# Performance work log

Hardware: AMD Instinct MI355X
Metric: run time of the kernel (lower is better)

Reference implementation:

```python
import jax, jax.numpy as jnp
import numpy as np

V = 25000
E = 100000
NODE_IN = 74
EDGE_IN = 12
OUT = 64
EHID = 128
NUM_STEPS = 6


def setup_inputs() -> dict:
    key = jax.random.key(0)
    ks = jax.random.split(key, 12)
    s = 0.05
    node_feats = jax.random.normal(ks[0], (V, NODE_IN), dtype=jnp.float32)
    edge_feats = jax.random.normal(ks[1], (E, EDGE_IN), dtype=jnp.float32)
    src = jax.random.randint(ks[2], (E,), 0, V)
    dst = jax.random.randint(ks[3], (E,), 0, V)
    # project_node_feats: Linear(node_in, out)
    Wp = jax.random.normal(ks[4], (NODE_IN, OUT), dtype=jnp.float32) * s
    bp = jnp.zeros((OUT,), dtype=jnp.float32)
    # edge network: Linear(edge_in, ehid) -> ReLU -> Linear(ehid, out*out)
    We1 = jax.random.normal(ks[5], (EDGE_IN, EHID), dtype=jnp.float32) * s
    be1 = jnp.zeros((EHID,), dtype=jnp.float32)
    We2 = jax.random.normal(ks[6], (EHID, OUT * OUT), dtype=jnp.float32) * s
    be2 = jnp.zeros((OUT * OUT,), dtype=jnp.float32)
    # NNConv output bias
    bias = jnp.zeros((OUT,), dtype=jnp.float32)
    return {
        "node_feats": node_feats, "edge_feats": edge_feats,
        "src": src, "dst": dst,
        "Wp": Wp, "bp": bp,
        "We1": We1, "be1": be1, "We2": We2, "be2": be2,
        "bias": bias,
    }


def reference(node_feats, edge_feats, src, dst, Wp, bp, We1, be1, We2, be2, bias):
    # project node features
    h = jax.nn.relu(node_feats @ Wp + bp)  # [V, OUT]
    # per-edge weight matrices (same every step -> hoist out of loop)
    ew = jax.nn.relu(edge_feats @ We1 + be1) @ We2 + be2  # [E, OUT*OUT]
    ew = ew.reshape(E, OUT, OUT)
    for _ in range(NUM_STEPS):
        # gather src node feats, batched matvec, scatter-sum to dst
        msg = jnp.einsum('ei,eio->eo', h[src], ew)  # [E, OUT]
        agg = jax.ops.segment_sum(msg, dst, num_segments=V)  # [V, OUT]
        h = jax.nn.relu(agg + bias)
    return h
```

## Files before the change

### kernel.cpp

```cpp
#include <hip/hip_runtime.h>
#include <hip/hip_bf16.h>

#define Vn 25000
#define En 100000
#define NODE_IN 74
#define EDGE_IN 12
#define OUTD 64
#define EHID 128
#define NUM_STEPS 6

typedef __attribute__((ext_vector_type(8))) _Float16 half8;
typedef __attribute__((ext_vector_type(2))) _Float16 half2v;
typedef __attribute__((ext_vector_type(4))) float floatx4;

__global__ void proj_kernel(const float* __restrict__ node,
                            const float* __restrict__ Wp,
                            const float* __restrict__ bp,
                            float* __restrict__ h) {
  __shared__ float nf[NODE_IN];
  int v = blockIdx.x;
  int o = threadIdx.x;
  for (int i = o; i < NODE_IN; i += 64) nf[i] = node[(size_t)v * NODE_IN + i];
  __syncthreads();
  float acc = bp[o];
  for (int i = 0; i < NODE_IN; ++i) acc = fmaf(nf[i], Wp[i * OUTD + o], acc);
  h[(size_t)v * OUTD + o] = fmaxf(acc, 0.0f);
}

__global__ void edge_kernel(const float* __restrict__ ef,
                            const float* __restrict__ We1,
                            const float* __restrict__ be1,
                            _Float16* __restrict__ f) {
  __shared__ float es[EDGE_IN];
  int e = blockIdx.x;
  int k = threadIdx.x;
  if (k < EDGE_IN) es[k] = ef[(size_t)e * EDGE_IN + k];
  __syncthreads();
  float acc = be1[k];
  for (int j = 0; j < EDGE_IN; ++j) acc = fmaf(es[j], We1[j * EHID + k], acc);
  f[(size_t)e * EHID + k] = (_Float16)fmaxf(acc, 0.0f);
}

__global__ void w2r_kernel(const float* __restrict__ We2,
                           _Float16* __restrict__ w2s) {
  int g = blockIdx.x * 256 + threadIdx.x;
  int j = g & 7;
  int quad = (g >> 3) & 3;
  int l15 = (g >> 5) & 15;
  int c = (g >> 9) & 3;
  int step = g >> 11;
  int s = step & 3;
  int i = step >> 2;
  int k = s * 32 + quad * 8 + j;
  int col = i * 64 + c * 16 + l15;
  int eidx = g & 2047;
  int estore = eidx ^ (((eidx >> 6) & 3) << 3);
  w2s[((size_t)step << 11) | estore] = (_Float16)We2[(size_t)k * (OUTD * OUTD) + col];
}

#define GLOAD_LDS(gp, lp)                                                     \
  __builtin_amdgcn_global_load_lds(                                           \
      (const __attribute__((address_space(1))) void*)(gp),                    \
      (__attribute__((address_space(3))) void*)(lp), 16, 0, 0)

__global__ __launch_bounds__(256, 3) void msg_kernel(
    const float* __restrict__ h,
    const _Float16* __restrict__ f,
    const _Float16* __restrict__ w2s,
    const int* __restrict__ src,
    const int* __restrict__ dst,
    const float* __restrict__ be2,
    float* __restrict__ agg) {
  __shared__ __align__(16) char smem_raw[49152];
  __shared__ int s_dst[128];

  const int tid = threadIdx.x;
  const int wv = tid >> 6;
  const int lane = tid & 63;
  const int quad = lane >> 4;
  const int l15 = lane & 15;
  const int e0 = blockIdx.x * 128;
  const int ew0 = e0 + wv * 32;

  _Float16* h16w = (_Float16*)(smem_raw + wv * 4096);
  char* ring = smem_raw + 16384;

  if (lane < 32) {
    int eg = ew0 + lane;
    s_dst[wv * 32 + lane] = (eg < En) ? dst[eg] : -1;
  }
  {
    int el = lane & 31;
    int ih = lane >> 5;
    int eg = ew0 + el;
    int sv = (eg < En) ? src[eg] : 0;
    const float4* hp = reinterpret_cast<const float4*>(h + (size_t)sv * OUTD + ih * 32);
    int pe = (el & 15) * 2 + (el >> 4);
#pragma unroll
    for (int c = 0; c < 8; ++c) {
      float4 v = hp[c];
      int i4 = ih * 32 + c * 4;
      h16w[(i4 + 0) * 32 + pe] = (_Float16)v.x;
      h16w[(i4 + 1) * 32 + pe] = (_Float16)v.y;
      h16w[(i4 + 2) * 32 + pe] = (_Float16)v.z;
      h16w[(i4 + 3) * 32 + pe] = (_Float16)v.w;
    }
  }

  half8 afr[2][4];
#pragma unroll
  for (int t = 0; t < 2; ++t) {
    int e = ew0 + t * 16 + l15;
    if (e >= En) e = En - 1;
    const _Float16* fr = f + (size_t)e * EHID + quad * 8;
#pragma unroll
    for (int s = 0; s < 4; ++s)
      afr[t][s] = *reinterpret_cast<const half8*>(fr + s * 32);
  }

  floatx4 acc[2][4];
  const floatx4 zero4 = (floatx4){0.f, 0.f, 0.f, 0.f};
#pragma unroll
  for (int t = 0; t < 2; ++t)
#pragma unroll
    for (int c = 0; c < 4; ++c) acc[t][c] = zero4;

  const char* w2b = (const char*)w2s;
  const int roff = l15 * 64 + ((quad ^ ((l15 >> 1) & 3)) << 4);
  const char* sp0 = ring + roff;
  const char* sp1 = ring + 4096 + roff;
  const char* sp2 = ring + 8192 + roff;
  const char* sp3 = ring + 12288 + roff;
  const char* sp4 = ring + 16384 + roff;
  const char* sp5 = ring + 20480 + roff;
  const char* sp6 = ring + 24576 + roff;
  const char* sp7 = ring + 28672 + roff;

#define STAGE1(GS, SLOT)                                                      \
  {                                                                           \
    const char* gp_ = w2b + (size_t)(GS) * 4096 + (wv << 10) + lane * 16;     \
    char* lp_ = ring + (SLOT) * 4096 + (wv << 10);                            \
    GLOAD_LDS(gp_, lp_);                                                      \
  }

  asm volatile("s_waitcnt vmcnt(0)" ::: "memory");

  STAGE1(0, 0);
  STAGE1(1, 1);
  STAGE1(2, 2);
  STAGE1(3, 3);
  STAGE1(4, 4);
  STAGE1(5, 5);
  STAGE1(6, 6);
  asm volatile("s_waitcnt vmcnt(6)" ::: "memory");
  asm volatile("s_barrier" ::: "memory");
  half8 P[4], Q[4];
  P[0] = *reinterpret_cast<const half8*>(sp0);
  P[1] = *reinterpret_cast<const half8*>(sp0 + 1024);
  P[2] = *reinterpret_cast<const half8*>(sp0 + 2048);
  P[3] = *reinterpret_cast<const half8*>(sp0 + 3072);

  half2v hv = *reinterpret_cast<const half2v*>(h16w + l15 * 2);
  half2v hvn;

#define KSTEP(SS, BMM, BRD, SPRD, STSL, GST)                                  \
  {                                                                           \
    asm volatile("s_waitcnt vmcnt(2)" ::: "memory");                          \
    asm volatile("s_barrier" ::: "memory");                                   \
    BRD[0] = *reinterpret_cast<const half8*>(SPRD);                           \
    BRD[1] = *reinterpret_cast<const half8*>(SPRD + 1024);                    \
    BRD[2] = *reinterpret_cast<const half8*>(SPRD + 2048);                    \
    BRD[3] = *reinterpret_cast<const half8*>(SPRD + 3072);                    \
    int gs_ = (GST) > 255 ? 255 : (GST);                                      \
    STAGE1(gs_, STSL);                                                        \
    __builtin_amdgcn_s_setprio(1);                                            \
    _Pragma("unroll") for (int t = 0; t < 2; ++t) {                           \
      half8 as = afr[t][SS] * hb[t];                                          \
      acc[t][0] = __builtin_amdgcn_mfma_f32_16x16x32_f16(as, BMM[0], acc[t][0], 0, 0, 0); \
      acc[t][1] = __builtin_amdgcn_mfma_f32_16x16x32_f16(as, BMM[1], acc[t][1], 0, 0, 0); \
      acc[t][2] = __builtin_amdgcn_mfma_f32_16x16x32_f16(as, BMM[2], acc[t][2], 0, 0, 0); \
      acc[t][3] = __builtin_amdgcn_mfma_f32_16x16x32_f16(as, BMM[3], acc[t][3], 0, 0, 0); \
    }                                                                         \
    __builtin_amdgcn_s_setprio(0);                                            \
  }

#define BUILD_HB(HSRC)                                                        \
  _Pragma("unroll") for (int t = 0; t < 2; ++t) {                             \
    _Float16 hf = (HSRC)[t];                                                  \
    hb[t] = (half8){hf, hf, hf, hf, hf, hf, hf, hf};                          \
  }

  for (int ip = 0; ip < 32; ++ip) {
    int g = ip * 8;
    half8 hb[2];
    BUILD_HB(hv);
    KSTEP(0, P, Q, sp1, 7, g + 7);
    hvn = *reinterpret_cast<const half2v*>(h16w + (2 * ip + 1) * 32 + l15 * 2);
    KSTEP(1, Q, P, sp2, 0, g + 8);
    KSTEP(2, P, Q, sp3, 1, g + 9);
    KSTEP(3, Q, P, sp4, 2, g + 10);
    BUILD_HB(hvn);
    KSTEP(0, P, Q, sp5, 3, g + 11);
    {
      int inx = (ip < 31) ? 2 * ip + 2 : 63;
      hv = *reinterpret_cast<const half2v*>(h16w + inx * 32 + l15 * 2);
    }
    KSTEP(1, Q, P, sp6, 4, g + 12);
    KSTEP(2, P, Q, sp7, 5, g + 13);
    KSTEP(3, Q, P, sp0, 6, g + 14);
  }

  asm volatile("s_waitcnt vmcnt(0)" ::: "memory");

  {
#pragma unroll
    for (int s = 0; s < 2; ++s) {
      half8 b2f[4];
#pragma unroll
      for (int c = 0; c < 4; ++c) {
        half8 v;
#pragma unroll
        for (int j = 0; j < 8; ++j)
          v[j] = (_Float16)be2[(s * 32 + quad * 8 + j) * 64 + c * 16 + l15];
        b2f[c] = v;
      }
#pragma unroll
      for (int t = 0; t < 2; ++t) {
        half8 ha;
#pragma unroll
        for (int j = 0; j < 8; ++j)
          ha[j] = h16w[(s * 32 + quad * 8 + j) * 32 + l15 * 2 + t];
#pragma unroll
        for (int c = 0; c < 4; ++c)
          acc[t][c] = __builtin_amdgcn_mfma_f32_16x16x32_f16(ha, b2f[c], acc[t][c], 0, 0, 0);
      }
    }
  }

#pragma unroll
  for (int t = 0; t < 2; ++t) {
    int rb = wv * 32 + t * 16 + quad * 4;
#pragma unroll
    for (int c = 0; c < 4; ++c) {
      int col = c * 16 + l15;
#pragma unroll
      for (int r = 0; r < 4; ++r) {
        int d = s_dst[rb + r];
        if (d >= 0) atomicAdd(&agg[(size_t)d * OUTD + col], acc[t][c][r]);
      }
    }
  }
}

__global__ void update_kernel(float* __restrict__ agg,
                              const float* __restrict__ bias,
                              float* __restrict__ hout,
                              float* __restrict__ dout, int last) {
  int g = blockIdx.x * 256 + threadIdx.x;
  if (g >= Vn * OUTD) return;
  float v = agg[g];
  agg[g] = 0.0f;
  float r = fmaxf(v + bias[g & 63], 0.0f);
  hout[g] = r;
  if (last) dout[g] = r;
}

extern "C" void kernel_launch(void* const* d_in, const int* in_sizes, int n_in,
                              void* d_out, int out_size, void* d_ws, size_t ws_size,
                              hipStream_t stream) {
  const float* node = (const float*)d_in[0];
  const float* edge = (const float*)d_in[1];
  const int* src = (const int*)d_in[2];
  const int* dst = (const int*)d_in[3];
  const float* Wp   = (const float*)d_in[4];
  const float* bp   = (const float*)d_in[5];
  const float* We1  = (const float*)d_in[6];
  const float* be1  = (const float*)d_in[7];
  const float* We2  = (const float*)d_in[8];
  const float* be2  = (const float*)d_in[9];
  const float* bias = (const float*)d_in[10];
  float* out = (float*)d_out;

  char* ws = (char*)d_ws;
  float* agg = (float*)(ws);
  float* h_a = (float*)(ws + 6400000);
  float* h_b = (float*)(ws + 12800000);
  _Float16* f   = (_Float16*)(ws + 19200000);
  _Float16* w2s = (_Float16*)(ws + 44800000);

  hipMemsetAsync(agg, 0, (size_t)Vn * OUTD * sizeof(float), stream);
  proj_kernel<<<Vn, 64, 0, stream>>>(node, Wp, bp, h_a);
  edge_kernel<<<En, 128, 0, stream>>>(edge, We1, be1, f);
  w2r_kernel<<<(OUTD * OUTD * EHID) / 256, 256, 0, stream>>>(We2, w2s);

  float* hin = h_a;
  float* hout = h_b;
  const int nblocks = (En + 127) / 128;
  for (int s = 0; s < NUM_STEPS; ++s) {
    msg_kernel<<<nblocks, 256, 0, stream>>>(hin, f, w2s, src, dst, be2, agg);
    update_kernel<<<(Vn * OUTD + 255) / 256, 256, 0, stream>>>(
        agg, bias, hout, out, s == NUM_STEPS - 1);
    float* t = hin; hin = hout; hout = t;
  }
}
```

Measured before the change: 940.2 us.

## Process two ring slots per barrier in edge-weight MFMA pipeline

Restructures the LDS ring pipeline so each barrier step reads two 4KB slots, issues two async global-to-LDS stages and runs two k-steps of MFMAs. This halves the number of s_waitcnt/s_barrier synchronisations per loop and gives the scheduler larger MFMA batches, with a sched_barrier to keep loads ahead of compute. The cost is more registers for the doubled B fragments and one less slot of prefetch depth. The vmcnt accounting changes to match (wait for 4 outstanding at startup, 2 per group).

```diff
diff --git a/kernel.cpp b/kernel.cpp
--- a/kernel.cpp
+++ b/kernel.cpp
@@ -143,6 +143,47 @@
     GLOAD_LDS(gp_, lp_);                                                      \
   }
 
+#define RD4(DST, SP)                                                          \
+  DST[0] = *reinterpret_cast<const half8*>(SP);                               \
+  DST[1] = *reinterpret_cast<const half8*>(SP + 1024);                        \
+  DST[2] = *reinterpret_cast<const half8*>(SP + 2048);                        \
+  DST[3] = *reinterpret_cast<const half8*>(SP + 3072);
+
+#define GROUP(SA, SBs, UA, UB, VA, VB, SPR1, SPR2, STS1, STS2, GS1, GS2)      \
+  {                                                                           \
+    asm volatile("s_waitcnt vmcnt(2)" ::: "memory");                          \
+    asm volatile("s_barrier" ::: "memory");                                   \
+    RD4(VA, SPR1);                                                            \
+    RD4(VB, SPR2);                                                            \
+    int g1_ = (GS1) > 255 ? 255 : (GS1);                                      \
+    int g2_ = (GS2) > 255 ? 255 : (GS2);                                      \
+    STAGE1(g1_, STS1);                                                        \
+    STAGE1(g2_, STS2);                                                        \
+    __builtin_amdgcn_sched_barrier(0);                                        \
+    __builtin_amdgcn_s_setprio(1);                                            \
+    _Pragma("unroll") for (int t = 0; t < 2; ++t) {                           \
+      half8 as = afr[t][SA] * hb[t];                                          \
+      acc[t][0] = __builtin_amdgcn_mfma_f32_16x16x32_f16(as, UA[0], acc[t][0], 0, 0, 0); \
+      acc[t][1] = __builtin_amdgcn_mfma_f32_16x16x32_f16(as, UA[1], acc[t][1], 0, 0, 0); \
+      acc[t][2] = __builtin_amdgcn_mfma_f32_16x16x32_f16(as, UA[2], acc[t][2], 0, 0, 0); \
+      acc[t][3] = __builtin_amdgcn_mfma_f32_16x16x32_f16(as, UA[3], acc[t][3], 0, 0, 0); \
+    }                                                                         \
+    _Pragma("unroll") for (int t = 0; t < 2; ++t) {                           \
+      half8 as = afr[t][SBs] * hb[t];                                         \
+      acc[t][0] = __builtin_amdgcn_mfma_f32_16x16x32_f16(as, UB[0], acc[t][0], 0, 0, 0); \
+      acc[t][1] = __builtin_amdgcn_mfma_f32_16x16x32_f16(as, UB[1], acc[t][1], 0, 0, 0); \
+      acc[t][2] = __builtin_amdgcn_mfma_f32_16x16x32_f16(as, UB[2], acc[t][2], 0, 0, 0); \
+      acc[t][3] = __builtin_amdgcn_mfma_f32_16x16x32_f16(as, UB[3], acc[t][3], 0, 0, 0); \
+    }                                                                         \
+    __builtin_amdgcn_s_setprio(0);                                            \
+  }
+
+#define BUILD_HB(HSRC)                                                        \
+  _Pragma("unroll") for (int t = 0; t < 2; ++t) {                             \
+    _Float16 hf = (HSRC)[t];                                                  \
+    hb[t] = (half8){hf, hf, hf, hf, hf, hf, hf, hf};                          \
+  }
+
   asm volatile("s_waitcnt vmcnt(0)" ::: "memory");
 
   STAGE1(0, 0);
@@ -151,63 +192,29 @@
   STAGE1(3, 3);
   STAGE1(4, 4);
   STAGE1(5, 5);
-  STAGE1(6, 6);
-  asm volatile("s_waitcnt vmcnt(6)" ::: "memory");
+  asm volatile("s_waitcnt vmcnt(4)" ::: "memory");
   asm volatile("s_barrier" ::: "memory");
-  half8 P[4], Q[4];
-  P[0] = *reinterpret_cast<const half8*>(sp0);
-  P[1] = *reinterpret_cast<const half8*>(sp0 + 1024);
-  P[2] = *reinterpret_cast<const half8*>(sp0 + 2048);
-  P[3] = *reinterpret_cast<const half8*>(sp0 + 3072);
+  half8 PA[4], PB[4], QA[4], QB[4];
+  RD4(PA, sp0);
+  RD4(PB, sp1);
 
   half2v hv = *reinterpret_cast<const half2v*>(h16w + l15 * 2);
   half2v hvn;
 
-#define KSTEP(SS, BMM, BRD, SPRD, STSL, GST)                                  \
-  {                                                                           \
-    asm volatile("s_waitcnt vmcnt(2)" ::: "memory");                          \
-    asm volatile("s_barrier" ::: "memory");                                   \
-    BRD[0] = *reinterpret_cast<const half8*>(SPRD);                           \
-    BRD[1] = *reinterpret_cast<const half8*>(SPRD + 1024);                    \
-    BRD[2] = *reinterpret_cast<const half8*>(SPRD + 2048);                    \
-    BRD[3] = *reinterpret_cast<const half8*>(SPRD + 3072);                    \
-    int gs_ = (GST) > 255 ? 255 : (GST);                                      \
-    STAGE1(gs_, STSL);                                                        \
-    __builtin_amdgcn_s_setprio(1);                                            \
-    _Pragma("unroll") for (int t = 0; t < 2; ++t) {                           \
-      half8 as = afr[t][SS] * hb[t];                                          \
-      acc[t][0] = __builtin_amdgcn_mfma_f32_16x16x32_f16(as, BMM[0], acc[t][0], 0, 0, 0); \
-      acc[t][1] = __builtin_amdgcn_mfma_f32_16x16x32_f16(as, BMM[1], acc[t][1], 0, 0, 0); \
-      acc[t][2] = __builtin_amdgcn_mfma_f32_16x16x32_f16(as, BMM[2], acc[t][2], 0, 0, 0); \
-      acc[t][3] = __builtin_amdgcn_mfma_f32_16x16x32_f16(as, BMM[3], acc[t][3], 0, 0, 0); \
-    }                                                                         \
-    __builtin_amdgcn_s_setprio(0);                                            \
-  }
-
-#define BUILD_HB(HSRC)                                                        \
-  _Pragma("unroll") for (int t = 0; t < 2; ++t) {                             \
-    _Float16 hf = (HSRC)[t];                                                  \
-    hb[t] = (half8){hf, hf, hf, hf, hf, hf, hf, hf};                          \
-  }
-
   for (int ip = 0; ip < 32; ++ip) {
-    int g = ip * 8;
+    int n = ip * 8;
     half8 hb[2];
     BUILD_HB(hv);
-    KSTEP(0, P, Q, sp1, 7, g + 7);
+    GROUP(0, 1, PA, PB, QA, QB, sp2, sp3, 6, 7, n + 6, n + 7);
     hvn = *reinterpret_cast<const half2v*>(h16w + (2 * ip + 1) * 32 + l15 * 2);
-    KSTEP(1, Q, P, sp2, 0, g + 8);
-    KSTEP(2, P, Q, sp3, 1, g + 9);
-    KSTEP(3, Q, P, sp4, 2, g + 10);
+    GROUP(2, 3, QA, QB, PA, PB, sp4, sp5, 0, 1, n + 8, n + 9);
     BUILD_HB(hvn);
-    KSTEP(0, P, Q, sp5, 3, g + 11);
+    GROUP(0, 1, PA, PB, QA, QB, sp6, sp7, 2, 3, n + 10, n + 11);
     {
-      int inx = (ip < 31) ? 2 * ip + 2 : 63;
+      int inx = (ip < 31) ? (2 * ip + 2) : 63;
       hv = *reinterpret_cast<const half2v*>(h16w + inx * 32 + l15 * 2);
     }
-    KSTEP(1, Q, P, sp6, 4, g + 12);
-    KSTEP(2, P, Q, sp7, 5, g + 13);
-    KSTEP(3, Q, P, sp0, 6, g + 14);
+    GROUP(2, 3, QA, QB, PA, PB, sp0, sp1, 4, 5, n + 12, n + 13);
   }
 
   asm volatile("s_waitcnt vmcnt(0)" ::: "memory");
```

Result: no change. 943.4 us (+0.3%).
